# Performance work log

Measured on AMD Instinct MI355X. Metric: run time of the kernel, lower is better.

Reference implementation:

```python
import jax, jax.numpy as jnp
import numpy as np

EMBED_DIM = 1024
NUM_HEADS = 16
HEAD_DIM = EMBED_DIM // NUM_HEADS


def setup_inputs() -> dict:
    key = jax.random.key(0)
    ks = jax.random.split(key, 6)
    std = 0.02
    x = jax.random.normal(ks[0], (2, 2048, EMBED_DIM), dtype=jnp.float32)
    Wq = jax.random.normal(ks[1], (EMBED_DIM, EMBED_DIM), dtype=jnp.float32) * std
    Wk = jax.random.normal(ks[2], (EMBED_DIM, EMBED_DIM), dtype=jnp.float32) * std
    Wv = jax.random.normal(ks[3], (EMBED_DIM, EMBED_DIM), dtype=jnp.float32) * std
    Wo = jax.random.normal(ks[4], (EMBED_DIM, EMBED_DIM), dtype=jnp.float32) * std
    Wf = jax.random.normal(ks[5], (NUM_HEADS, EMBED_DIM), dtype=jnp.float32) * std
    return {"x": x, "Wq": Wq, "Wk": Wk, "Wv": Wv, "Wo": Wo, "Wf": Wf}


def reference(x, Wq, Wk, Wv, Wo, Wf):
    b, n, d = x.shape
    h, hd = NUM_HEADS, HEAD_DIM
    # projections (nn.Linear without bias: y = x @ W^T)
    q = (x @ Wq.T).reshape(b, n, h, hd)
    k = (x @ Wk.T).reshape(b, n, h, hd)
    v = (x @ Wv.T).reshape(b, n, h, hd)
    # per-head log forget gate and its causal cumulative sum
    log_f = jax.nn.log_sigmoid(x @ Wf.T)          # [b, n, h]
    c = jnp.cumsum(log_f, axis=1)                 # [b, n, h], c_i = sum_{t<=i} log f_t
    cbh = c.transpose(0, 2, 1)                    # [b, h, n]
    scale = 1.0 / np.sqrt(hd).astype(np.float32)
    # scores s_ij = q_i.k_j * scale + (c_i - c_j)  (decay D_ij = sum_{t=j+1}^i log f_t)
    scores = jnp.einsum("bihd,bjhd->bhij", q, k) * scale
    scores = scores + cbh[:, :, :, None] - cbh[:, :, None, :]
    causal = jnp.tril(jnp.ones((n, n), dtype=bool))
    scores = jnp.where(causal, scores, -1e30)
    p = jax.nn.softmax(scores, axis=-1)           # [b, h, n, n]
    out = jnp.einsum("bhij,bjhd->bihd", p, v).reshape(b, n, d)
    return out @ Wo.T
```

## Files before the change

### kernel.cpp

```cpp
#include <hip/hip_runtime.h>

#define EMBED 1024
#define NHEAD 16
#define HD    64
#define SEQ   2048
#define BATCH 2
#define ROWS  (BATCH * SEQ)

typedef float f32x4 __attribute__((ext_vector_type(4)));
typedef short short8 __attribute__((ext_vector_type(8)));
typedef short short4v __attribute__((ext_vector_type(4)));
typedef unsigned short u16x4 __attribute__((ext_vector_type(4)));
typedef unsigned short u16x8 __attribute__((ext_vector_type(8)));
typedef unsigned u32x4 __attribute__((ext_vector_type(4)));
typedef unsigned u32x2 __attribute__((ext_vector_type(2)));

#define LOG2E 1.4426950408889634f

__device__ __forceinline__ unsigned short f2bf(float f) {
  unsigned int u = __builtin_bit_cast(unsigned int, f);
  u += 0x7fffu + ((u >> 16) & 1u);
  return (unsigned short)(u >> 16);
}

__device__ __forceinline__ unsigned cvtpk(float lo, float hi) {
  unsigned r;
  asm("v_cvt_pk_bf16_f32 %0, %1, %2" : "=v"(r) : "v"(lo), "v"(hi));
  return r;
}

#if __has_builtin(__builtin_amdgcn_exp2f)
#define EXP2(x) __builtin_amdgcn_exp2f(x)
#else
#define EXP2(x) exp2f(x)
#endif

__device__ __forceinline__ void gll16(const void* g, const void* l) {
  __builtin_amdgcn_global_load_lds(
      (const __attribute__((address_space(1))) unsigned int*)g,
      (__attribute__((address_space(3))) unsigned int*)l, 16, 0, 0);
}

__device__ __forceinline__ unsigned lds_addr(const void* p) {
  return (unsigned)(size_t)(__attribute__((address_space(3))) const void*)p;
}

__global__ __launch_bounds__(256) void cvt_all_kernel(
    const float* __restrict__ x,
    const float* __restrict__ w0, const float* __restrict__ w1,
    const float* __restrict__ w2, const float* __restrict__ w3,
    const float* __restrict__ wf,
    unsigned short* __restrict__ xo, unsigned short* __restrict__ xlo,
    unsigned short* __restrict__ o0, unsigned short* __restrict__ o1,
    unsigned short* __restrict__ o2, unsigned short* __restrict__ o3,
    unsigned short* __restrict__ wfh, unsigned short* __restrict__ wfl,
    unsigned* __restrict__ qkmaxu) {
  const int y = blockIdx.y;
  if (y < 4) {
    const float* in = (y == 0) ? w0 : (y == 1) ? w1 : (y == 2) ? w2 : w3;
    unsigned short* out = (y == 0) ? o0 : (y == 1) ? o1 : (y == 2) ? o2 : o3;
    const int i = blockIdx.x * 256 + threadIdx.x;
    f32x4 v = reinterpret_cast<const f32x4*>(in)[i];
    u16x4 o;
#pragma unroll
    for (int e = 0; e < 4; ++e) o[e] = f2bf(v[e]);
    reinterpret_cast<u16x4*>(out)[i] = o;
  } else if (y == 4) {
    const int i0 = blockIdx.x * 256 + threadIdx.x;
#pragma unroll
    for (int e = 0; e < 4; ++e) {
      const int i = i0 + e * 262144;
      f32x4 v = reinterpret_cast<const f32x4*>(x)[i];
      u16x4 h, l;
#pragma unroll
      for (int q = 0; q < 4; ++q) {
        h[q] = f2bf(v[q]);
        const float hf = __builtin_bit_cast(float, (unsigned)h[q] << 16);
        l[q] = f2bf(v[q] - hf);
      }
      reinterpret_cast<u16x4*>(xo)[i] = h;
      reinterpret_cast<u16x4*>(xlo)[i] = l;
    }
  } else {
    if (blockIdx.x < 16) {
      const int i = blockIdx.x * 256 + threadIdx.x;
      f32x4 v = reinterpret_cast<const f32x4*>(wf)[i];
      u16x4 h, l;
#pragma unroll
      for (int q = 0; q < 4; ++q) {
        h[q] = f2bf(v[q]);
        const float hf = __builtin_bit_cast(float, (unsigned)h[q] << 16);
        l[q] = f2bf(v[q] - hf);
      }
      reinterpret_cast<u16x4*>(wfh)[i] = h;
      reinterpret_cast<u16x4*>(wfl)[i] = l;
    } else if (blockIdx.x == 16) {
      if (threadIdx.x < 64) qkmaxu[threadIdx.x] = 0u;
    }
  }
}

__global__ __launch_bounds__(256) void gemm_wo_kernel(
    const unsigned short* __restrict__ A, const unsigned short* __restrict__ B,
    float* __restrict__ C) {
  __shared__ unsigned short Asm[64 * 64];
  __shared__ unsigned short Bsm[128 * 64];
  const int tid = threadIdx.x, wid = tid >> 6, lane = tid & 63;
  const int g = lane >> 4, l16 = lane & 15;
  const int wr = wid >> 1, wc = wid & 1;
  const int mb = blockIdx.y;
  const int nb = blockIdx.x;

  f32x4 acc[2][4] = {};

  for (int k0 = 0; k0 < EMBED; k0 += 64) {
    __syncthreads();
#pragma unroll
    for (int q = 0; q < 2; ++q) {
      const int base = (wid * 2 + q) * 1024;
      const int off = base + lane * 16;
      const int row = off >> 7;
      const int colel = (off & 127) >> 1;
      gll16(A + (size_t)(mb * 64 + row) * EMBED + k0 + colel, (const char*)Asm + base);
    }
#pragma unroll
    for (int q = 0; q < 4; ++q) {
      const int base = (wid * 4 + q) * 1024;
      const int off = base + lane * 16;
      const int row = off >> 7;
      const int colel = (off & 127) >> 1;
      gll16(B + (size_t)(nb * 128 + row) * EMBED + k0 + colel, (const char*)Bsm + base);
    }
    __syncthreads();

#pragma unroll
    for (int kc = 0; kc < 2; ++kc) {
      short8 am[2], bm[4];
#pragma unroll
      for (int mi = 0; mi < 2; ++mi)
        am[mi] = *reinterpret_cast<const short8*>(&Asm[(wr * 32 + mi * 16 + l16) * 64 + kc * 32 + g * 8]);
#pragma unroll
      for (int ni = 0; ni < 4; ++ni)
        bm[ni] = *reinterpret_cast<const short8*>(&Bsm[(wc * 64 + ni * 16 + l16) * 64 + kc * 32 + g * 8]);
#pragma unroll
      for (int mi = 0; mi < 2; ++mi)
#pragma unroll
        for (int ni = 0; ni < 4; ++ni)
          acc[mi][ni] = __builtin_amdgcn_mfma_f32_16x16x32_bf16(am[mi], bm[ni], acc[mi][ni], 0, 0, 0);
    }
  }

#pragma unroll
  for (int mi = 0; mi < 2; ++mi)
#pragma unroll
    for (int ni = 0; ni < 4; ++ni)
#pragma unroll
      for (int r = 0; r < 4; ++r) {
        const int m = mb * 64 + wr * 32 + mi * 16 + g * 4 + r;
        const int n = nb * 128 + wc * 64 + ni * 16 + l16;
        C[(size_t)m * EMBED + n] = acc[mi][ni][r];
      }
}

#define BAR() asm volatile("s_barrier" ::: "memory")
#define LGKM0()                                              \
  do {                                                       \
    asm volatile("s_waitcnt lgkmcnt(0)" ::: "memory");       \
    __builtin_amdgcn_sched_barrier(0);                       \
  } while (0)
#define VM(n_) asm volatile("s_waitcnt vmcnt(" #n_ ")" ::: "memory")

template <bool OUT_BF16>
__global__ __launch_bounds__(512, 2) void gemm256_kernel(
    const unsigned short* __restrict__ A,
    const unsigned short* __restrict__ B0, const unsigned short* __restrict__ B1,
    const unsigned short* __restrict__ B2,
    void* __restrict__ C0, void* __restrict__ C1, void* __restrict__ C2,
    unsigned* __restrict__ qkmaxu) {
  __shared__ unsigned short sm[2][2][2][8192];
  const int tid = threadIdx.x, wid = tid >> 6, lane = tid & 63;
  const int g = lane >> 4, l16 = lane & 15;
  const int wr = wid >> 2, wcol = wid & 3;
  const int mb = blockIdx.y;
  const int nb = blockIdx.x;
  const int which = nb >> 2;
  const int col0 = (nb & 3) * 256;
  const unsigned short* Bp = (which == 0) ? B0 : (which == 1) ? B1 : B2;
  void* Cp = (which == 0) ? C0 : (which == 1) ? C1 : C2;

  const int lane8 = lane & 7, laneHi = lane >> 3;
  const int colel = (lane8 ^ laneHi) * 8;
  int soff[2];
#pragma unroll
  for (int q = 0; q < 2; ++q)
    soff[q] = (q * 64 + wid * 8 + laneHi) * EMBED + colel;
  const unsigned short* Ag = A + (size_t)(mb * 256) * EMBED;
  const unsigned short* Bg = Bp + (size_t)col0 * EMBED;

  const int sw = (l16 & 7) << 4;
  const int cs0 = (0 | (g * 16)) ^ sw;
  const int cs1 = (64 | (g * 16)) ^ sw;
  const char* smB = (const char*)sm;
  const int aBase = wr * 16384 + l16 * 128;
  const int bBase = 32768 + (wcol >> 1) * 16384 + (wcol & 1) * 8192 + l16 * 128;

#define STG(buf_, ab_, half_, gsrc_, t_)                                               \
  do {                                                                                 \
    const unsigned short* gp_ = (gsrc_) + (size_t)(half_) * (128 * EMBED) + (t_) * 64; \
    char* lp_ = (char*)sm + (buf_) * 65536 + (ab_) * 32768 + (half_) * 16384 + wid * 1024; \
    gll16(gp_ + soff[0], lp_);                                                         \
    gll16(gp_ + soff[1], lp_ + 8192);                                                  \
  } while (0)

#define RD_A(buf_, row_, kc_) \
  (*reinterpret_cast<const short8*>(smB + (buf_) * 65536 + aBase + (row_) * 2048 + ((kc_) ? cs1 : cs0)))
#define RD_B(buf_, row_, kc_) \
  (*reinterpret_cast<const short8*>(smB + (buf_) * 65536 + bBase + (row_) * 2048 + ((kc_) ? cs1 : cs0)))

#define QUAD(mg_, ng_)                                                                   \
  do {                                                                                   \
    __builtin_amdgcn_s_setprio(1);                                                       \
    _Pragma("unroll") for (int kc_ = 0; kc_ < 2; ++kc_)                                  \
      _Pragma("unroll") for (int mi_ = 0; mi_ < 4; ++mi_)                                \
        _Pragma("unroll") for (int nj_ = 0; nj_ < 2; ++nj_)                              \
          acc[(mg_) * 4 + mi_][(ng_) * 2 + nj_] = __builtin_amdgcn_mfma_f32_16x16x32_bf16( \
              fa[mi_][kc_], fb[(ng_) * 2 + nj_][kc_], acc[(mg_) * 4 + mi_][(ng_) * 2 + nj_], 0, 0, 0); \
    __builtin_amdgcn_s_setprio(0);                                                       \
  } while (0)

#define KTILE4(BUF_, STG_P1, STG_P2, STG_P3, STG_P4_VM)                                  \
  do {                                                                                   \
    _Pragma("unroll") for (int mi_ = 0; mi_ < 4; ++mi_) {                                \
      fa[mi_][0] = RD_A(BUF_, mi_, 0);                                                   \
      fa[mi_][1] = RD_A(BUF_, mi_, 1);                                                   \
    }                                                                                    \
    _Pragma("unroll") for (int ni_ = 0; ni_ < 2; ++ni_) {                                \
      fb[ni_][0] = RD_B(BUF_, ni_, 0);                                                   \
      fb[ni_][1] = RD_B(BUF_, ni_, 1);                                                   \
    }                                                                                    \
    STG_P1;                                                                              \
    asm volatile("s_waitcnt lgkmcnt(8)" ::: "memory");                                   \
    BAR();                                                                               \
    LGKM0();                                                                             \
    QUAD(0, 0);                                                                          \
    BAR();                                                                               \
    _Pragma("unroll") for (int ni_ = 0; ni_ < 2; ++ni_) {                                \
      fb[2 + ni_][0] = RD_B(BUF_, 2 + ni_, 0);                                           \
      fb[2 + ni_][1] = RD_B(BUF_, 2 + ni_, 1);                                           \
    }                                                                                    \
    STG_P2;                                                                              \
    BAR();                                                                               \
    LGKM0();                                                                             \
    QUAD(0, 1);                                                                          \
    BAR();                                                                               \
    _Pragma("unroll") for (int mi_ = 0; mi_ < 4; ++mi_) {                                \
      fa[mi_][0] = RD_A(BUF_, 4 + mi_, 0);                                               \
      fa[mi_][1] = RD_A(BUF_, 4 + mi_, 1);                                               \
    }                                                                                    \
    STG_P3;                                                                              \
    BAR();                                                                               \
    LGKM0();                                                                             \
    QUAD(1, 0);                                                                          \
    BAR();                                                                               \
    STG_P4_VM;                                                                           \
    BAR();                                                                               \
    QUAD(1, 1);                                                                          \
    BAR();                                                                               \
  } while (0)

  short8 fa[4][2], fb[4][2];
  f32x4 acc[8][4] = {};

  STG(0, 0, 0, Ag, 0);
  STG(0, 1, 0, Bg, 0);
  STG(0, 0, 1, Ag, 0);
  STG(0, 1, 1, Bg, 0);
  STG(1, 1, 0, Bg, 1);
  STG(1, 1, 1, Bg, 1);
  VM(4);
  BAR();

  for (int it = 0; it < 8; ++it) {
    const int t1 = 2 * it + 1, t2 = 2 * it + 2, t3 = 2 * it + 3;
    const bool nl = (it < 7);
    KTILE4(0,
           STG(1, 0, 0, Ag, t1),
           STG(1, 0, 1, Ag, t1),
           if (nl) STG(0, 1, 0, Bg, t2),
           if (nl) { STG(0, 1, 1, Bg, t2); VM(4); } else VM(0));
    KTILE4(1,
           if (nl) STG(0, 0, 0, Ag, t2),
           if (nl) STG(0, 0, 1, Ag, t2),
           if (nl) STG(1, 1, 0, Bg, t3),
           if (nl) { STG(1, 1, 1, Bg, t3); VM(4); });
  }

  unsigned mxv = 0;
#pragma unroll
  for (int mi = 0; mi < 8; ++mi)
#pragma unroll
    for (int ni = 0; ni < 4; ++ni)
#pragma unroll
      for (int r = 0; r < 4; ++r) {
        const int m = mb * 256 + wr * 128 + mi * 16 + g * 4 + r;
        const int n = col0 + wcol * 64 + ni * 16 + l16;
        if (OUT_BF16) {
          const unsigned short bv = f2bf(acc[mi][ni][r]);
          ((unsigned short*)Cp)[(size_t)m * EMBED + n] = bv;
          const unsigned a = bv & 0x7fffu;
          mxv = a > mxv ? a : mxv;
        } else {
          ((float*)Cp)[(size_t)m * EMBED + n] = acc[mi][ni][r];
        }
      }
  if (OUT_BF16 && which < 2) {
#pragma unroll
    for (int mm = 1; mm < 64; mm <<= 1) {
      const unsigned o = __shfl_xor(mxv, mm);
      mxv = o > mxv ? o : mxv;
    }
    if (lane == 0) {
      const int bbat = (mb >= 8) ? 1 : 0;
      const int head = (nb & 3) * 4 + wcol;
      const int idx = which * 32 + bbat * 16 + head;
      atomicMax(&qkmaxu[idx], mxv << 16);
    }
  }
#undef STG
#undef RD_A
#undef RD_B
#undef QUAD
#undef KTILE4
}
#undef BAR
#undef LGKM0
#undef VM

__global__ __launch_bounds__(256) void gate_kernel(
    const unsigned short* __restrict__ xh, const unsigned short* __restrict__ xl,
    const unsigned short* __restrict__ wh, const unsigned short* __restrict__ wl,
    float* __restrict__ c) {
  __shared__ f32x4 red[4][64];
  const int tid = threadIdx.x, wid = tid >> 6, lane = tid & 63;
  const int g = lane >> 4, l16 = lane & 15;
  const int row0 = blockIdx.x * 16;
  const int k0 = wid * 256;
  const unsigned short* xhp = xh + (size_t)(row0 + l16) * EMBED + k0 + g * 8;
  const unsigned short* xlp = xl + (size_t)(row0 + l16) * EMBED + k0 + g * 8;
  const unsigned short* whp = wh + (size_t)l16 * EMBED + k0 + g * 8;
  const unsigned short* wlp = wl + (size_t)l16 * EMBED + k0 + g * 8;
  f32x4 acc = {};
#pragma unroll
  for (int k = 0; k < 8; ++k) {
    const short8 ah = *reinterpret_cast<const short8*>(xhp + k * 32);
    const short8 al = *reinterpret_cast<const short8*>(xlp + k * 32);
    const short8 bh = *reinterpret_cast<const short8*>(whp + k * 32);
    const short8 bl = *reinterpret_cast<const short8*>(wlp + k * 32);
    acc = __builtin_amdgcn_mfma_f32_16x16x32_bf16(ah, bh, acc, 0, 0, 0);
    acc = __builtin_amdgcn_mfma_f32_16x16x32_bf16(ah, bl, acc, 0, 0, 0);
    acc = __builtin_amdgcn_mfma_f32_16x16x32_bf16(al, bh, acc, 0, 0, 0);
  }
  red[wid][lane] = acc;
  __syncthreads();
  if (wid == 0) {
    const f32x4 a = red[0][lane] + red[1][lane] + red[2][lane] + red[3][lane];
#pragma unroll
    for (int r = 0; r < 4; ++r) {
      const float s = a[r];
      const float ls = (fminf(s, 0.f) - log1pf(__expf(-fabsf(s)))) * LOG2E;
      const int n = row0 + g * 4 + r;
      const int b = n >> 11, nn = n & (SEQ - 1);
      c[(size_t)(b * NHEAD + l16) * SEQ + nn] = ls;
    }
  }
}

__global__ void cumsum_kernel(float* __restrict__ c) {
  const int bh = blockIdx.x;
  const int lane = threadIdx.x;
  float* p = c + (size_t)bh * SEQ;
  f32x4 vv[8];
  f32x4* vp = reinterpret_cast<f32x4*>(p + lane * 32);
#pragma unroll
  for (int q = 0; q < 8; ++q) vv[q] = vp[q];
  float run = 0.f;
#pragma unroll
  for (int q = 0; q < 8; ++q)
#pragma unroll
    for (int e = 0; e < 4; ++e) { run += vv[q][e]; vv[q][e] = run; }
  float s = run;
#pragma unroll
  for (int off = 1; off < 64; off <<= 1) {
    float u = __shfl_up(s, off);
    if (lane >= off) s += u;
  }
  const float excl = s - run;
#pragma unroll
  for (int q = 0; q < 8; ++q)
#pragma unroll
    for (int e = 0; e < 4; ++e) vv[q][e] += excl;
#pragma unroll
  for (int q = 0; q < 8; ++q) vp[q] = vv[q];
}

#define NINF (-3.0e38f)
#define SCL (0.125f * LOG2E)
#define BMARG 14.0f

#define TR_READ(dst, addr, OFF) \
  asm volatile("ds_read_b64_tr_b16 %0, %1 offset:" OFF : "=v"(dst) : "v"(addr))

__global__ __launch_bounds__(256) void fa_attn_kernel(
    const unsigned short* __restrict__ Q, const unsigned short* __restrict__ K,
    const unsigned short* __restrict__ V, const float* __restrict__ C,
    const float* __restrict__ qkmax, unsigned short* __restrict__ O) {
  __shared__ unsigned short Ksm[2][4096];
  __shared__ unsigned short Vsm[2][4096];
  const int p = blockIdx.x;
  const int xcd = p & 7, s2 = p >> 3;
  const int hb = xcd * 4 + (s2 >> 5);
  const int qb = s2 & 31;
  const int hh = hb & 15, bb = hb >> 4;
  const int tid = threadIdx.x, wid = tid >> 6, lane = tid & 63;
  const int g = lane >> 4, l16 = lane & 15;
  const int i_base = qb * 64 + wid * 16;

  const float* cptr = C + (size_t)(bb * NHEAD + hh) * SEQ;

  int kOff[2], vOff[2];
#pragma unroll
  for (int qq = 0; qq < 2; ++qq) {
    const int q = wid * 2 + qq;
    {
      const int row = q * 8 + (lane >> 3);
      const int colel = ((lane & 7) ^ (lane >> 3)) * 8;
      kOff[qq] = row * EMBED + colel;
    }
    {
      const int dblk = q >> 1;
      const int j = (q & 1) * 32 + (lane >> 1);
      const int dlow = (lane & 1) * 8;
      vOff[qq] = j * EMBED + dblk * 16 + dlow;
    }
  }
  const unsigned short* Kbase = K + (size_t)bb * SEQ * EMBED + hh * HD;
  const unsigned short* Vbase = V + (size_t)bb * SEQ * EMBED + hh * HD;

  const int swz = (l16 & 7) << 4;
  const int koffB0 = ((0) | (g * 16)) ^ swz;
  const int koffB1 = ((64) | (g * 16)) ^ swz;
  const int krowB = l16 * 128;

#define STAGE(bufidx, tt)                                                              \
  do {                                                                                 \
    const unsigned short* kb_ = Kbase + (size_t)(tt) * 64 * EMBED;                     \
    const unsigned short* vb_ = Vbase + (size_t)(tt) * 64 * EMBED;                     \
    _Pragma("unroll") for (int qq = 0; qq < 2; ++qq) {                                 \
      gll16(kb_ + kOff[qq], (const char*)&Ksm[bufidx][0] + (wid * 2 + qq) * 1024);     \
      gll16(vb_ + vOff[qq], (const char*)&Vsm[bufidx][0] + (wid * 2 + qq) * 1024);     \
    }                                                                                  \
  } while (0)

  short8 qf0, qf1;
  {
    const unsigned short* qp = Q + (size_t)(bb * SEQ + i_base + l16) * EMBED + hh * HD + g * 8;
    qf0 = *reinterpret_cast<const short8*>(qp);
    qf1 = *reinterpret_cast<const short8*>(qp + 32);
  }
  const float c2i = cptr[i_base + l16];

  int t_start = qb;
  {
    const float qm = qkmax[hb];
    const float km = qkmax[32 + hb];
    const float thr = -41.f - 23.0832f * qm * km;
    const float c2imin = cptr[qb * 64];
    while (t_start > 0 && (c2imin - cptr[t_start * 64 - 1] >= thr)) --t_start;
  }

  float mc_prev = (t_start == qb) ? c2i : cptr[t_start * 64 + 63];
  float l_ = 0.f;
  f32x4 accd[4] = {};

  STAGE(0, t_start);
  __syncthreads();

  int buf = 0;
  for (int t = t_start; t <= qb; ++t) {
    if (t < qb) STAGE(buf ^ 1, t + 1);
    const int kv0 = t * 64;
    const bool diag = (t == qb);
    const int nj = diag ? (wid + 1) : 4;

    const float mc_cur = diag ? c2i : cptr[kv0 + 63];
    const float corr = EXP2(mc_cur - mc_prev);
    mc_prev = mc_cur;
    const float mcB = mc_cur - BMARG;

    float pf[4][4];
    float lsum = 0.f;
#pragma unroll
    for (int jb = 0; jb < 4; ++jb) {
      if (jb < nj) {
        const char* kbp = (const char*)&Ksm[buf][0] + jb * 2048 + krowB;
        short8 kf0 = *reinterpret_cast<const short8*>(kbp + koffB0);
        short8 kf1 = *reinterpret_cast<const short8*>(kbp + koffB1);
        f32x4 s = {};
        __builtin_amdgcn_s_setprio(1);
        s = __builtin_amdgcn_mfma_f32_16x16x32_bf16(kf0, qf0, s, 0, 0, 0);
        s = __builtin_amdgcn_mfma_f32_16x16x32_bf16(kf1, qf1, s, 0, 0, 0);
        __builtin_amdgcn_s_setprio(0);
        const f32x4 cv = *reinterpret_cast<const f32x4*>(&cptr[kv0 + jb * 16 + g * 4]);
#pragma unroll
        for (int r = 0; r < 4; ++r) {
          float arg = __builtin_fmaf(s[r], SCL, mcB - cv[r]);
          if (diag && jb == wid && (g * 4 + r > l16)) arg = NINF;
          const float pv = EXP2(arg);
          pf[jb][r] = pv;
          lsum += pv;
        }
      } else {
#pragma unroll
        for (int r = 0; r < 4; ++r) pf[jb][r] = 0.f;
      }
    }
    l_ = l_ * corr + lsum;
#pragma unroll
    for (int d = 0; d < 4; ++d) accd[d] *= corr;

    u32x4 w0, w1;
    w0[0] = cvtpk(pf[0][0], pf[0][1]); w0[1] = cvtpk(pf[0][2], pf[0][3]);
    w0[2] = cvtpk(pf[1][0], pf[1][1]); w0[3] = cvtpk(pf[1][2], pf[1][3]);
    w1[0] = cvtpk(pf[2][0], pf[2][1]); w1[1] = cvtpk(pf[2][2], pf[2][3]);
    w1[2] = cvtpk(pf[3][0], pf[3][1]); w1[3] = cvtpk(pf[3][2], pf[3][3]);
    const short8 pb0 = __builtin_bit_cast(short8, w0);
    const short8 pb1 = __builtin_bit_cast(short8, w1);

    const unsigned vb0 = lds_addr(&Vsm[buf][0]) + lane * 8;
#pragma unroll
    for (int db = 0; db < 4; ++db) {
      const unsigned va = vb0 + db * 2048;
      short4v t0, t1, t2, t3;
      TR_READ(t0, va, "0");
      TR_READ(t1, va, "512");
      TR_READ(t2, va, "1024");
      TR_READ(t3, va, "1536");
      asm volatile("s_waitcnt lgkmcnt(0)" ::: "memory");
      __builtin_amdgcn_sched_barrier(0);
      short8 va0, va1;
#pragma unroll
      for (int e = 0; e < 4; ++e) {
        va0[e] = t0[e]; va0[e + 4] = t1[e];
        va1[e] = t2[e]; va1[e + 4] = t3[e];
      }
      __builtin_amdgcn_s_setprio(1);
      accd[db] = __builtin_amdgcn_mfma_f32_16x16x32_bf16(va0, pb0, accd[db], 0, 0, 0);
      accd[db] = __builtin_amdgcn_mfma_f32_16x16x32_bf16(va1, pb1, accd[db], 0, 0, 0);
      __builtin_amdgcn_s_setprio(0);
    }
    __syncthreads();
    buf ^= 1;
  }

  l_ += __shfl_xor(l_, 16);
  l_ += __shfl_xor(l_, 32);
  const float inv = 1.0f / l_;
  unsigned short* op = O + (size_t)(bb * SEQ + i_base + l16) * EMBED + hh * HD;
#pragma unroll
  for (int db = 0; db < 4; ++db) {
    u32x2 o;
    o[0] = cvtpk(accd[db][0] * inv, accd[db][1] * inv);
    o[1] = cvtpk(accd[db][2] * inv, accd[db][3] * inv);
    *reinterpret_cast<u32x2*>(op + db * 16 + g * 4) = o;
  }
#undef STAGE
}

extern "C" void kernel_launch(void* const* d_in, const int* in_sizes, int n_in,
                              void* d_out, int out_size, void* d_ws, size_t ws_size,
                              hipStream_t stream) {
  const float* x = (const float*)d_in[0];
  const float* Wq = (const float*)d_in[1];
  const float* Wk = (const float*)d_in[2];
  const float* Wv = (const float*)d_in[3];
  const float* Wo = (const float*)d_in[4];
  const float* Wf = (const float*)d_in[5];
  float* out = (float*)d_out;

  char* ws = (char*)d_ws;
  const size_t SZ_X = (size_t)ROWS * EMBED * sizeof(unsigned short);
  const size_t SZ_W = (size_t)EMBED * EMBED * sizeof(unsigned short);
  const size_t SZ_WF = (size_t)NHEAD * EMBED * sizeof(unsigned short);
  unsigned short* xb = (unsigned short*)ws;   ws += SZ_X;
  unsigned short* xlo = (unsigned short*)ws;  ws += SZ_X;
  unsigned short* Wqb = (unsigned short*)ws;  ws += SZ_W;
  unsigned short* Wkb = (unsigned short*)ws;  ws += SZ_W;
  unsigned short* Wvb = (unsigned short*)ws;  ws += SZ_W;
  unsigned short* Wob = (unsigned short*)ws;  ws += SZ_W;
  unsigned short* Wfh = (unsigned short*)ws;  ws += SZ_WF;
  unsigned short* Wfl = (unsigned short*)ws;  ws += SZ_WF;
  unsigned short* Qb = (unsigned short*)ws;   ws += SZ_X;
  unsigned short* Kb = (unsigned short*)ws;   ws += SZ_X;
  unsigned short* Vb = (unsigned short*)ws;   ws += SZ_X;
  unsigned short* attnb = (unsigned short*)ws; ws += SZ_X;
  float* carr = (float*)ws;                   ws += (size_t)BATCH * NHEAD * SEQ * sizeof(float);
  float* qkmax = (float*)ws;                  ws += 64 * sizeof(float);

  cvt_all_kernel<<<dim3(1024, 6), 256, 0, stream>>>(
      x, Wq, Wk, Wv, Wo, Wf, xb, xlo, Wqb, Wkb, Wvb, Wob, Wfh, Wfl,
      (unsigned*)qkmax);

  gate_kernel<<<256, 256, 0, stream>>>(xb, xlo, Wfh, Wfl, carr);

  gemm256_kernel<true><<<dim3(12, 16), 512, 0, stream>>>(
      xb, Wqb, Wkb, Wvb, Qb, Kb, Vb, (unsigned*)qkmax);

  cumsum_kernel<<<BATCH * NHEAD, 64, 0, stream>>>(carr);

  fa_attn_kernel<<<1024, 256, 0, stream>>>(Qb, Kb, Vb, carr, qkmax, attnb);

  gemm_wo_kernel<<<dim3(8, 64), 256, 0, stream>>>(attnb, Wob, out);
}
```

Baseline: 96.27 us.

## Retile QKV GEMM to 128x384 blocks for better CU occupancy

Reshapes the fused QKV projection GEMM from 256x256 tiles (192 blocks) to 128x384 tiles spanning the concatenated Q/K/V output (256 blocks). Each wave computes 64x96, and the staging, fragment loads and MFMA schedule are rewritten to match. The per-head max-abs tracking now splits across two heads per wave. The aim is to fill more of the 256 CUs and reduce wave-quantization tail. The cost is lower arithmetic intensity per tile, since there are more A reloads per output.

```diff
diff --git a/kernel.cpp b/kernel.cpp
--- a/kernel.cpp
+++ b/kernel.cpp
@@ -170,23 +170,18 @@
   } while (0)
 #define VM(n_) asm volatile("s_waitcnt vmcnt(" #n_ ")" ::: "memory")
 
-template <bool OUT_BF16>
-__global__ __launch_bounds__(512, 2) void gemm256_kernel(
+__global__ __launch_bounds__(512, 2) void gemm_qkv_kernel(
     const unsigned short* __restrict__ A,
     const unsigned short* __restrict__ B0, const unsigned short* __restrict__ B1,
     const unsigned short* __restrict__ B2,
-    void* __restrict__ C0, void* __restrict__ C1, void* __restrict__ C2,
-    unsigned* __restrict__ qkmaxu) {
-  __shared__ unsigned short sm[2][2][2][8192];
+    unsigned short* __restrict__ C0, unsigned short* __restrict__ C1,
+    unsigned short* __restrict__ C2, unsigned* __restrict__ qkmaxu) {
+  __shared__ unsigned short sm[2][32768];
   const int tid = threadIdx.x, wid = tid >> 6, lane = tid & 63;
   const int g = lane >> 4, l16 = lane & 15;
   const int wr = wid >> 2, wcol = wid & 3;
   const int mb = blockIdx.y;
   const int nb = blockIdx.x;
-  const int which = nb >> 2;
-  const int col0 = (nb & 3) * 256;
-  const unsigned short* Bp = (which == 0) ? B0 : (which == 1) ? B1 : B2;
-  void* Cp = (which == 0) ? C0 : (which == 1) ? C1 : C2;
 
   const int lane8 = lane & 7, laneHi = lane >> 3;
   const int colel = (lane8 ^ laneHi) * 8;
@@ -194,143 +189,148 @@
 #pragma unroll
   for (int q = 0; q < 2; ++q)
     soff[q] = (q * 64 + wid * 8 + laneHi) * EMBED + colel;
-  const unsigned short* Ag = A + (size_t)(mb * 256) * EMBED;
-  const unsigned short* Bg = Bp + (size_t)col0 * EMBED;
+  const unsigned short* Ag = A + (size_t)(mb * 128) * EMBED;
+  const unsigned short* bsrc[3];
+#pragma unroll
+  for (int c = 0; c < 3; ++c) {
+    const int k = 3 * nb + c;
+    const unsigned short* mp = ((k >> 3) == 0) ? B0 : ((k >> 3) == 1) ? B1 : B2;
+    bsrc[c] = mp + (size_t)((k & 7) * 128) * EMBED;
+  }
 
   const int sw = (l16 & 7) << 4;
   const int cs0 = (0 | (g * 16)) ^ sw;
   const int cs1 = (64 | (g * 16)) ^ sw;
   const char* smB = (const char*)sm;
-  const int aBase = wr * 16384 + l16 * 128;
-  const int bBase = 32768 + (wcol >> 1) * 16384 + (wcol & 1) * 8192 + l16 * 128;
-
-#define STG(buf_, ab_, half_, gsrc_, t_)                                               \
-  do {                                                                                 \
-    const unsigned short* gp_ = (gsrc_) + (size_t)(half_) * (128 * EMBED) + (t_) * 64; \
-    char* lp_ = (char*)sm + (buf_) * 65536 + (ab_) * 32768 + (half_) * 16384 + wid * 1024; \
-    gll16(gp_ + soff[0], lp_);                                                         \
-    gll16(gp_ + soff[1], lp_ + 8192);                                                  \
+  const int aOff = (wr * 64 + l16) * 128;
+  const int bOff = 16384 + (wcol * 96 + l16) * 128;
+
+#define STGU(buf_, uoff_, gsrc_, t_)                                       \
+  do {                                                                     \
+    const unsigned short* gp_ = (gsrc_) + (size_t)(t_) * 64;               \
+    char* lp_ = (char*)sm + (buf_) * 65536 + (uoff_) + wid * 1024;         \
+    gll16(gp_ + soff[0], lp_);                                             \
+    gll16(gp_ + soff[1], lp_ + 8192);                                      \
   } while (0)
 
-#define RD_A(buf_, row_, kc_) \
-  (*reinterpret_cast<const short8*>(smB + (buf_) * 65536 + aBase + (row_) * 2048 + ((kc_) ? cs1 : cs0)))
-#define RD_B(buf_, row_, kc_) \
-  (*reinterpret_cast<const short8*>(smB + (buf_) * 65536 + bBase + (row_) * 2048 + ((kc_) ? cs1 : cs0)))
-
-#define QUAD(mg_, ng_)                                                                   \
+#define RD_A(buf_, mi_, kc_) \
+  (*reinterpret_cast<const short8*>(smB + (buf_) * 65536 + aOff + (mi_) * 2048 + ((kc_) ? cs1 : cs0)))
+#define RD_B(buf_, ni_, kc_) \
+  (*reinterpret_cast<const short8*>(smB + (buf_) * 65536 + bOff + (ni_) * 2048 + ((kc_) ? cs1 : cs0)))
+
+#define QUADN(kc_, nh_)                                                                  \
   do {                                                                                   \
     __builtin_amdgcn_s_setprio(1);                                                       \
-    _Pragma("unroll") for (int kc_ = 0; kc_ < 2; ++kc_)                                  \
-      _Pragma("unroll") for (int mi_ = 0; mi_ < 4; ++mi_)                                \
-        _Pragma("unroll") for (int nj_ = 0; nj_ < 2; ++nj_)                              \
-          acc[(mg_) * 4 + mi_][(ng_) * 2 + nj_] = __builtin_amdgcn_mfma_f32_16x16x32_bf16( \
-              fa[mi_][kc_], fb[(ng_) * 2 + nj_][kc_], acc[(mg_) * 4 + mi_][(ng_) * 2 + nj_], 0, 0, 0); \
+    _Pragma("unroll") for (int mi_ = 0; mi_ < 4; ++mi_)                                  \
+      _Pragma("unroll") for (int nj_ = 0; nj_ < 3; ++nj_)                                \
+        acc[mi_][(nh_) * 3 + nj_] = __builtin_amdgcn_mfma_f32_16x16x32_bf16(             \
+            fa[mi_], fb[(nh_) * 3 + nj_][kc_], acc[mi_][(nh_) * 3 + nj_], 0, 0, 0);      \
     __builtin_amdgcn_s_setprio(0);                                                       \
   } while (0)
 
-#define KTILE4(BUF_, STG_P1, STG_P2, STG_P3, STG_P4_VM)                                  \
+#define KT(BUF_, SA_, SB0_, SB1_, SB2VM_)                                                \
   do {                                                                                   \
-    _Pragma("unroll") for (int mi_ = 0; mi_ < 4; ++mi_) {                                \
-      fa[mi_][0] = RD_A(BUF_, mi_, 0);                                                   \
-      fa[mi_][1] = RD_A(BUF_, mi_, 1);                                                   \
-    }                                                                                    \
-    _Pragma("unroll") for (int ni_ = 0; ni_ < 2; ++ni_) {                                \
+    _Pragma("unroll") for (int mi_ = 0; mi_ < 4; ++mi_) fa[mi_] = RD_A(BUF_, mi_, 0);    \
+    _Pragma("unroll") for (int ni_ = 0; ni_ < 6; ++ni_) {                                \
       fb[ni_][0] = RD_B(BUF_, ni_, 0);                                                   \
       fb[ni_][1] = RD_B(BUF_, ni_, 1);                                                   \
     }                                                                                    \
-    STG_P1;                                                                              \
+    SA_;                                                                                 \
     asm volatile("s_waitcnt lgkmcnt(8)" ::: "memory");                                   \
     BAR();                                                                               \
     LGKM0();                                                                             \
-    QUAD(0, 0);                                                                          \
-    BAR();                                                                               \
-    _Pragma("unroll") for (int ni_ = 0; ni_ < 2; ++ni_) {                                \
-      fb[2 + ni_][0] = RD_B(BUF_, 2 + ni_, 0);                                           \
-      fb[2 + ni_][1] = RD_B(BUF_, 2 + ni_, 1);                                           \
-    }                                                                                    \
-    STG_P2;                                                                              \
+    QUADN(0, 0);                                                                         \
+    BAR();                                                                               \
+    SB0_;                                                                                \
+    BAR();                                                                               \
+    QUADN(0, 1);                                                                         \
+    BAR();                                                                               \
+    _Pragma("unroll") for (int mi_ = 0; mi_ < 4; ++mi_) fa[mi_] = RD_A(BUF_, mi_, 1);    \
+    SB1_;                                                                                \
     BAR();                                                                               \
     LGKM0();                                                                             \
-    QUAD(0, 1);                                                                          \
-    BAR();                                                                               \
-    _Pragma("unroll") for (int mi_ = 0; mi_ < 4; ++mi_) {                                \
-      fa[mi_][0] = RD_A(BUF_, 4 + mi_, 0);                                               \
-      fa[mi_][1] = RD_A(BUF_, 4 + mi_, 1);                                               \
-    }                                                                                    \
-    STG_P3;                                                                              \
-    BAR();                                                                               \
-    LGKM0();                                                                             \
-    QUAD(1, 0);                                                                          \
-    BAR();                                                                               \
-    STG_P4_VM;                                                                           \
-    BAR();                                                                               \
-    QUAD(1, 1);                                                                          \
+    QUADN(1, 0);                                                                         \
+    BAR();                                                                               \
+    SB2VM_;                                                                              \
+    BAR();                                                                               \
+    QUADN(1, 1);                                                                         \
     BAR();                                                                               \
   } while (0)
 
-  short8 fa[4][2], fb[4][2];
-  f32x4 acc[8][4] = {};
-
-  STG(0, 0, 0, Ag, 0);
-  STG(0, 1, 0, Bg, 0);
-  STG(0, 0, 1, Ag, 0);
-  STG(0, 1, 1, Bg, 0);
-  STG(1, 1, 0, Bg, 1);
-  STG(1, 1, 1, Bg, 1);
-  VM(4);
+  short8 fa[4], fb[6][2];
+  f32x4 acc[4][6] = {};
+
+  STGU(0, 0, Ag, 0);
+  STGU(0, 16384, bsrc[0], 0);
+  STGU(0, 32768, bsrc[1], 0);
+  STGU(0, 49152, bsrc[2], 0);
+  STGU(1, 16384, bsrc[0], 1);
+  STGU(1, 32768, bsrc[1], 1);
+  STGU(1, 49152, bsrc[2], 1);
+  VM(6);
   BAR();
 
   for (int it = 0; it < 8; ++it) {
     const int t1 = 2 * it + 1, t2 = 2 * it + 2, t3 = 2 * it + 3;
     const bool nl = (it < 7);
-    KTILE4(0,
-           STG(1, 0, 0, Ag, t1),
-           STG(1, 0, 1, Ag, t1),
-           if (nl) STG(0, 1, 0, Bg, t2),
-           if (nl) { STG(0, 1, 1, Bg, t2); VM(4); } else VM(0));
-    KTILE4(1,
-           if (nl) STG(0, 0, 0, Ag, t2),
-           if (nl) STG(0, 0, 1, Ag, t2),
-           if (nl) STG(1, 1, 0, Bg, t3),
-           if (nl) { STG(1, 1, 1, Bg, t3); VM(4); });
-  }
-
-  unsigned mxv = 0;
-#pragma unroll
-  for (int mi = 0; mi < 8; ++mi)
-#pragma unroll
-    for (int ni = 0; ni < 4; ++ni)
+    KT(0,
+       STGU(1, 0, Ag, t1),
+       if (nl) STGU(0, 16384, bsrc[0], t2),
+       if (nl) STGU(0, 32768, bsrc[1], t2),
+       if (nl) { STGU(0, 49152, bsrc[2], t2); VM(4); } else VM(0));
+    KT(1,
+       if (nl) STGU(0, 0, Ag, t2),
+       if (nl) STGU(1, 16384, bsrc[0], t3),
+       if (nl) STGU(1, 32768, bsrc[1], t3),
+       if (nl) { STGU(1, 49152, bsrc[2], t3); VM(4); });
+  }
+
+  unsigned mx0 = 0, mx1 = 0;
+  const int hshift = (wcol * 96) >> 6;
+#pragma unroll
+  for (int mi = 0; mi < 4; ++mi)
+#pragma unroll
+    for (int ni = 0; ni < 6; ++ni) {
+      const int nbase = nb * 384 + wcol * 96 + ni * 16;
+      const int which = nbase >> 10;
+      unsigned short* Cp = (which == 0) ? C0 : (which == 1) ? C1 : C2;
+      const int coll = (nbase & 1023) + l16;
+      const int hl = ((wcol * 96 + ni * 16) >> 6) - hshift;
+      unsigned mloc = 0;
 #pragma unroll
       for (int r = 0; r < 4; ++r) {
-        const int m = mb * 256 + wr * 128 + mi * 16 + g * 4 + r;
-        const int n = col0 + wcol * 64 + ni * 16 + l16;
-        if (OUT_BF16) {
-          const unsigned short bv = f2bf(acc[mi][ni][r]);
-          ((unsigned short*)Cp)[(size_t)m * EMBED + n] = bv;
-          const unsigned a = bv & 0x7fffu;
-          mxv = a > mxv ? a : mxv;
-        } else {
-          ((float*)Cp)[(size_t)m * EMBED + n] = acc[mi][ni][r];
-        }
+        const int m = mb * 128 + wr * 64 + mi * 16 + g * 4 + r;
+        const unsigned short bv = f2bf(acc[mi][ni][r]);
+        Cp[(size_t)m * EMBED + coll] = bv;
+        const unsigned a = bv & 0x7fffu;
+        mloc = a > mloc ? a : mloc;
       }
-  if (OUT_BF16 && which < 2) {
-#pragma unroll
-    for (int mm = 1; mm < 64; mm <<= 1) {
-      const unsigned o = __shfl_xor(mxv, mm);
-      mxv = o > mxv ? o : mxv;
-    }
-    if (lane == 0) {
-      const int bbat = (mb >= 8) ? 1 : 0;
-      const int head = (nb & 3) * 4 + wcol;
-      const int idx = which * 32 + bbat * 16 + head;
-      atomicMax(&qkmaxu[idx], mxv << 16);
-    }
-  }
-#undef STG
+      if (hl) mx1 = mloc > mx1 ? mloc : mx1;
+      else    mx0 = mloc > mx0 ? mloc : mx0;
+    }
+#pragma unroll
+  for (int mm = 1; mm < 64; mm <<= 1) {
+    const unsigned o0 = __shfl_xor(mx0, mm);
+    mx0 = o0 > mx0 ? o0 : mx0;
+    const unsigned o1 = __shfl_xor(mx1, mm);
+    mx1 = o1 > mx1 ? o1 : mx1;
+  }
+  if (lane == 0) {
+    const int bbat = (mb >= 16) ? 1 : 0;
+    const int hbase = (nb * 384 + wcol * 96) >> 6;
+#pragma unroll
+    for (int i = 0; i < 2; ++i) {
+      const int hg = hbase + i;
+      const int tens = hg >> 4;
+      if (tens < 2)
+        atomicMax(&qkmaxu[tens * 32 + bbat * 16 + (hg & 15)], (i ? mx1 : mx0) << 16);
+    }
+  }
+#undef STGU
 #undef RD_A
 #undef RD_B
-#undef QUAD
-#undef KTILE4
+#undef QUADN
+#undef KT
 }
 #undef BAR
 #undef LGKM0
@@ -612,7 +612,7 @@
 
   gate_kernel<<<256, 256, 0, stream>>>(xb, xlo, Wfh, Wfl, carr);
 
-  gemm256_kernel<true><<<dim3(12, 16), 512, 0, stream>>>(
+  gemm_qkv_kernel<<<dim3(8, 32), 512, 0, stream>>>(
       xb, Wqb, Wkb, Wvb, Qb, Kb, Vb, (unsigned*)qkmax);
 
   cumsum_kernel<<<BATCH * NHEAD, 64, 0, stream>>>(carr);
```

Measured after the change: 101.3 us. 1.05x slower.
